# Kernel optimization log

Hardware: AMD Instinct MI355X
Metric: run time of the kernel (lower is better)

The kernel has to match this reference:

```python
import jax, jax.numpy as jnp
import numpy as np

C, H = 256, 256  # feat_num, feat_h (equirect is H x 2H)


def setup_inputs() -> dict:
    key = jax.random.key(0)
    ks = jax.random.split(key, 6)
    m = jax.random.normal(ks[0], (1, C, H, 2 * H), jnp.float32)
    b = jax.random.normal(ks[1], (1, C, H, H), jnp.float32)
    u = jax.random.normal(ks[2], (1, C, H, H), jnp.float32)
    d = jax.random.normal(ks[3], (1, C, H, H), jnp.float32)
    Wf = jax.random.normal(ks[4], (C, C, 3, 3), jnp.float32) * 0.02
    bf = jnp.zeros((C,), jnp.float32)
    Wm = jax.random.normal(ks[5], (1, 2 * C, 1, 1), jnp.float32) * 0.02
    bm = jnp.zeros((1,), jnp.float32)
    return {"m": m, "b": b, "u": u, "d": d, "Wf": Wf, "bf": bf, "Wm": Wm, "bm": bm}


def _cube2equi(cube, out_h, out_w):
    # cube: [6, C, h, h]; face order: 0 back(z-), 1 down(y-), 2 front(z+), 3 left(x-), 4 right(x+), 5 up(y+)
    h = cube.shape[-1]
    theta = (jnp.arange(out_w, dtype=cube.dtype) + 0.5) / out_w * (2.0 * jnp.pi) - jnp.pi  # longitude [-pi, pi)
    phi = jnp.pi / 2 - (jnp.arange(out_h, dtype=cube.dtype) + 0.5) / out_h * jnp.pi        # latitude [pi/2, -pi/2]
    st, ct = jnp.sin(theta)[None, :], jnp.cos(theta)[None, :]
    sp, cp = jnp.sin(phi)[:, None], jnp.cos(phi)[:, None]
    dx = cp * st
    dy = jnp.broadcast_to(sp, (out_h, out_w))
    dz = cp * ct
    ax, ay, az = jnp.abs(dx), jnp.abs(dy), jnp.abs(dz)
    mx = jnp.maximum(jnp.maximum(ax, ay), az)
    px, py, pz = dx / mx, dy / mx, dz / mx
    cond_z = (az >= ax) & (az >= ay)
    cond_x = (~cond_z) & (ax >= ay)
    face = jnp.where(cond_z, jnp.where(dz > 0, 2, 0),
           jnp.where(cond_x, jnp.where(dx > 0, 4, 3),
                              jnp.where(dy > 0, 5, 1)))
    a = jnp.where(cond_z, jnp.where(dz > 0, px, -px),
        jnp.where(cond_x, jnp.where(dx > 0, -pz, pz), px))
    bcoord = jnp.where(cond_z | cond_x, -py, jnp.where(dy > 0, pz, -pz))
    uu = jnp.clip((a + 1.0) * 0.5 * (h - 1), 0.0, h - 1)
    vv = jnp.clip((bcoord + 1.0) * 0.5 * (h - 1), 0.0, h - 1)
    u0 = jnp.floor(uu).astype(jnp.int32); v0 = jnp.floor(vv).astype(jnp.int32)
    u1 = jnp.minimum(u0 + 1, h - 1); v1 = jnp.minimum(v0 + 1, h - 1)
    wu = uu - u0; wv = vv - v0

    def samp(vi, ui):
        return cube[face, :, vi, ui]  # [out_h, out_w, C] gather over all channels

    out = (samp(v0, u0) * ((1 - wv) * (1 - wu))[..., None]
         + samp(v0, u1) * ((1 - wv) * wu)[..., None]
         + samp(v1, u0) * (wv * (1 - wu))[..., None]
         + samp(v1, u1) * (wv * wu)[..., None])
    return jnp.transpose(out, (2, 0, 1))  # [C, out_h, out_w]


def _conv(x, w, bias, pad):
    y = jax.lax.conv_general_dilated(x, w, (1, 1), [(pad, pad), (pad, pad)],
                                     dimension_numbers=("NCHW", "OIHW", "NCHW"))
    return y + bias[None, :, None, None]


def reference(m, b, u, d, Wf, bf, Wm, bm):
    h = b.shape[-1]
    empty = jnp.zeros_like(b[0])  # the torch module's zero 'emptyFace' parameter
    # faces stacked as [back, down, empty, empty, empty, up], vectorized over all channels
    cube = jnp.stack([b[0], d[0], empty, empty, empty, u[0]])  # [6, C, h, h]
    aux = _cube2equi(cube, h, 2 * h)[None]                      # [1, C, h, 2h]
    M_aux = jax.nn.relu(_conv(aux, Wf, bf, 1))
    M_main = jax.nn.relu(_conv(m, Wf, bf, 1))
    mask = jax.nn.sigmoid(_conv(jnp.concatenate([M_main, M_aux], axis=1), Wm, bm, 0))
    return m + mask * M_aux
```

## Files before the change

### kernel.cpp

```cpp
#include <hip/hip_runtime.h>
#include <hip/hip_bf16.h>

#define NPIX 131072
#define WP   514
#define XP_BYTES 67897344
#define XP_STRIDE 67962880
#define FT_BYTES 100663296

typedef __attribute__((ext_vector_type(8))) short bf16x8;
typedef __attribute__((ext_vector_type(4))) float f32x4;

typedef const __attribute__((address_space(1))) void g_cvoid;
typedef __attribute__((address_space(3))) void l_void;

__device__ __forceinline__ void async16(const void* g, void* l) {
  __builtin_amdgcn_global_load_lds((g_cvoid*)g, (l_void*)l, 16, 0, 0);
}

__global__ void zero_borders(__hip_bfloat16* Xm, __hip_bfloat16* Xa) {
  int i = blockIdx.x;
  __hip_bfloat16* X = blockIdx.y ? Xa : Xm;
  long ppix;
  if (i < 514)       ppix = i;
  else if (i < 1028) ppix = 257L * WP + (i - 514);
  else if (i < 1284) ppix = (long)(i - 1028 + 1) * WP;
  else               ppix = (long)(i - 1284 + 1) * WP + 513;
  ((unsigned int*)(X + ppix * 256))[threadIdx.x] = 0u;
}

__global__ void zero_mask(float* maskacc) {
  maskacc[blockIdx.x * 256 + threadIdx.x] = 0.f;
}

__global__ void prep_weights(const float* __restrict__ Wf, __hip_bfloat16* __restrict__ Wtt) {
  int idx = blockIdx.x * 256 + threadIdx.x;
  int cout = idx / 2304, rem = idx % 2304;
  int o = rem >> 8, ci = rem & 255;
  Wtt[(((o << 5) + (ci >> 3)) << 11) + (cout << 3) + (ci & 7)] =
      __float2bfloat16(Wf[(cout * 256 + ci) * 9 + o]);
}

__global__ void nchw_to_pad_nhwc(const float* __restrict__ src, __hip_bfloat16* __restrict__ Xp) {
  __shared__ __align__(16) __hip_bfloat16 tile[64 * 264];
  int tid = threadIdx.x;
  int p0 = blockIdx.x * 64;
  int px = tid & 63, w = tid >> 6;
  for (int k = 0; k < 64; ++k) {
    int c = (k << 2) + w;
    tile[px * 264 + c] = __float2bfloat16(src[(long)c * NPIX + p0 + px]);
  }
  __syncthreads();
  int y = p0 >> 9, x0 = p0 & 511;
  long basep = (long)(y + 1) * WP + x0 + 1;
  for (int pass = 0; pass < 8; ++pass) {
    int tpx = (pass << 3) + (tid >> 5);
    int chunk = tid & 31;
    uint4 v = *(const uint4*)&tile[tpx * 264 + (chunk << 3)];
    *(uint4*)&Xp[(basep + tpx) * 256 + (chunk << 3)] = v;
  }
}

__global__ void face_to_nhwc(const float* __restrict__ fb, const float* __restrict__ fd,
                             const float* __restrict__ fu, __hip_bfloat16* __restrict__ Ft) {
  __shared__ __align__(16) __hip_bfloat16 tile[64 * 264];
  int tid = threadIdx.x;
  int face = blockIdx.x >> 10;
  int p0 = (blockIdx.x & 1023) << 6;
  const float* src = (face == 0) ? fb : (face == 1) ? fd : fu;
  int px = tid & 63, w = tid >> 6;
  for (int k = 0; k < 64; ++k) {
    int c = (k << 2) + w;
    tile[px * 264 + c] = __float2bfloat16(src[(long)c * 65536 + p0 + px]);
  }
  __syncthreads();
  long basep = ((long)face << 16) + p0;
  for (int pass = 0; pass < 8; ++pass) {
    int tpx = (pass << 3) + (tid >> 5);
    int chunk = tid & 31;
    uint4 v = *(const uint4*)&tile[tpx * 264 + (chunk << 3)];
    *(uint4*)&Ft[((basep + tpx) << 8) + (chunk << 3)] = v;
  }
}

__device__ __forceinline__ void bf8_fma(uint4 q, float w, float* acc) {
  unsigned x;
  x = q.x; acc[0] += w * __uint_as_float(x << 16); acc[1] += w * __uint_as_float(x & 0xffff0000u);
  x = q.y; acc[2] += w * __uint_as_float(x << 16); acc[3] += w * __uint_as_float(x & 0xffff0000u);
  x = q.z; acc[4] += w * __uint_as_float(x << 16); acc[5] += w * __uint_as_float(x & 0xffff0000u);
  x = q.w; acc[6] += w * __uint_as_float(x << 16); acc[7] += w * __uint_as_float(x & 0xffff0000u);
}

__global__ void aux_gen_v2(const __hip_bfloat16* __restrict__ Ft,
                           __hip_bfloat16* __restrict__ Xp) {
  const int lane = threadIdx.x & 63;
  const int p = (blockIdx.x << 2) + (threadIdx.x >> 6);
  const int yy = p >> 9, xx = p & 511;

  float theta = ((xx + 0.5f) / 512.f) * 6.283185307179586f - 3.141592653589793f;
  float phi   = 1.5707963267948966f - ((yy + 0.5f) / 256.f) * 3.141592653589793f;
  float st = sinf(theta), ct = cosf(theta);
  float sp = sinf(phi),   cp = cosf(phi);
  float dx = cp * st, dy = sp, dz = cp * ct;
  float ax = fabsf(dx), ay = fabsf(dy), az = fabsf(dz);
  float mx = fmaxf(fmaxf(ax, ay), az);
  float pxn = dx / mx, pyn = dy / mx, pzn = dz / mx;
  bool cz = (az >= ax) && (az >= ay);
  bool cx = (!cz) && (ax >= ay);
  int face; float a, b;
  if (cz)      { face = dz > 0.f ? 2 : 0; a = dz > 0.f ? pxn : -pxn; b = -pyn; }
  else if (cx) { face = dx > 0.f ? 4 : 3; a = dx > 0.f ? -pzn : pzn; b = -pyn; }
  else         { face = dy > 0.f ? 5 : 1; a = pxn; b = dy > 0.f ? pzn : -pzn; }
  float uu = fminf(fmaxf((a + 1.f) * 0.5f * 255.f, 0.f), 255.f);
  float vv = fminf(fmaxf((b + 1.f) * 0.5f * 255.f, 0.f), 255.f);

  const long outbase = ((long)((yy + 1) * WP + xx + 1)) << 8;
  const int c0 = (lane >> 1) << 3;
  const int up = lane & 1;
  const int slot = (face == 0) ? 0 : (face == 1) ? 1 : (face == 5) ? 2 : -1;

  if (slot < 0) {
    if (!up) *(uint4*)&Xp[outbase + c0] = make_uint4(0u, 0u, 0u, 0u);
    return;
  }
  int u0 = (int)uu, v0 = (int)vv;
  int u1 = min(u0 + 1, 255), v1 = min(v0 + 1, 255);
  float wu = uu - (float)u0, wv = vv - (float)v0;
  int uc = up ? u1 : u0;
  float wA = up ? wu : (1.f - wu);
  const __hip_bfloat16* base = Ft + ((long)slot << 24);

  float acc[8] = {0.f, 0.f, 0.f, 0.f, 0.f, 0.f, 0.f, 0.f};
  uint4 q0 = *(const uint4*)&base[(((long)(v0 << 8) + uc) << 8) + c0];
  uint4 q1 = *(const uint4*)&base[(((long)(v1 << 8) + uc) << 8) + c0];
  bf8_fma(q0, (1.f - wv) * wA, acc);
  bf8_fma(q1, wv * wA, acc);
#pragma unroll
  for (int j = 0; j < 8; ++j) acc[j] += __shfl_xor(acc[j], 1);
  if (!up) {
    union { uint4 q; __hip_bfloat16 h[8]; } o;
#pragma unroll
    for (int j = 0; j < 8; ++j) o.h[j] = __float2bfloat16(acc[j]);
    *(uint4*)&Xp[outbase + c0] = o.q;
  }
}

__global__ void aux_gen(const float* __restrict__ fb, const float* __restrict__ fd,
                        const float* __restrict__ fu,
                        __hip_bfloat16* __restrict__ Xp) {
  __shared__ __align__(16) __hip_bfloat16 tile[64 * 264];
  int tid = threadIdx.x;
  int p0 = blockIdx.x * 64;
  int px = tid & 63, w = tid >> 6;

  int p = p0 + px;
  int yy = p >> 9, xx = p & 511;
  float theta = ((xx + 0.5f) / 512.f) * 6.283185307179586f - 3.141592653589793f;
  float phi   = 1.5707963267948966f - ((yy + 0.5f) / 256.f) * 3.141592653589793f;
  float st = sinf(theta), ct = cosf(theta);
  float sp = sinf(phi),   cp = cosf(phi);
  float dx = cp * st, dy = sp, dz = cp * ct;
  float ax = fabsf(dx), ay = fabsf(dy), az = fabsf(dz);
  float mx = fmaxf(fmaxf(ax, ay), az);
  float pxn = dx / mx, pyn = dy / mx, pzn = dz / mx;
  bool cz = (az >= ax) && (az >= ay);
  bool cx = (!cz) && (ax >= ay);
  int face; float a, b;
  if (cz)      { face = dz > 0.f ? 2 : 0; a = dz > 0.f ? pxn : -pxn; b = -pyn; }
  else if (cx) { face = dx > 0.f ? 4 : 3; a = dx > 0.f ? -pzn : pzn; b = -pyn; }
  else         { face = dy > 0.f ? 5 : 1; a = pxn; b = dy > 0.f ? pzn : -pzn; }
  float uu = fminf(fmaxf((a + 1.f) * 0.5f * 255.f, 0.f), 255.f);
  float vv = fminf(fmaxf((b + 1.f) * 0.5f * 255.f, 0.f), 255.f);

  const float* F = (face == 0) ? fb : (face == 1) ? fd : (face == 5) ? fu : nullptr;
  int u0 = (int)uu, v0 = (int)vv;
  int u1 = min(u0 + 1, 255), v1 = min(v0 + 1, 255);
  float wu = uu - (float)u0, wv = vv - (float)v0;
  float w00 = (1.f - wv) * (1.f - wu), w01 = (1.f - wv) * wu;
  float w10 = wv * (1.f - wu),         w11 = wv * wu;
  int i00 = v0 * 256 + u0, i01 = v0 * 256 + u1;
  int i10 = v1 * 256 + u0, i11 = v1 * 256 + u1;
  for (int k = 0; k < 64; ++k) {
    int c = (k << 2) + w;
    float val = 0.f;
    if (F) {
      const float* Fc = F + ((long)c << 16);
      val = w00 * Fc[i00] + w01 * Fc[i01] + w10 * Fc[i10] + w11 * Fc[i11];
    }
    tile[px * 264 + c] = __float2bfloat16(val);
  }
  __syncthreads();
  int y = p0 >> 9, x0g = p0 & 511;
  long basep = (long)(y + 1) * WP + x0g + 1;
  for (int pass = 0; pass < 8; ++pass) {
    int tpx = (pass << 3) + (tid >> 5);
    int chunk = tid & 31;
    uint4 v = *(const uint4*)&tile[tpx * 264 + (chunk << 3)];
    *(uint4*)&Xp[(basep + tpx) * 256 + (chunk << 3)] = v;
  }
}

template <bool STORE>
__global__ void conv3x3_mfma(const __hip_bfloat16* __restrict__ Xp,
                             const __hip_bfloat16* __restrict__ Wtt,
                             const float* __restrict__ bias,
                             const float* __restrict__ wm,
                             __hip_bfloat16* __restrict__ Out,
                             float* __restrict__ maskacc) {
  __shared__ __align__(16) __hip_bfloat16 At[4 * 80 * 32];
  const int tid = threadIdx.x;
  const int wave = tid >> 6, lane = tid & 63;
  const int bx = blockIdx.x;
  const int n0 = (bx & 1) << 7;
  const int tile = bx >> 1;
  const int x0 = (tile >> 7) << 6;
  const int y0 = (tile & 127) << 1;
  const int wrow = wave >> 1;
  const int n_off = (wave & 1) << 6;
  const int lq = lane >> 4, ln = lane & 15;

  const long stage_row = (long)(y0 + wave) * WP + x0;
  const int s_col = lane >> 2;
  const int s_ci  = (lane & 3) << 3;

  f32x4 acc[4][4] = {};

  for (int s = 0; s < 8; ++s) {
    const int ci0 = s << 5;
#pragma unroll
    for (int j = 0; j < 5; ++j) {
      const __hip_bfloat16* gp = Xp + ((stage_row + (j << 4) + s_col) << 8) + ci0 + s_ci;
      async16(gp, &At[(wave * 80 + (j << 4)) << 5]);
    }
    __syncthreads();
#pragma unroll
    for (int o = 0; o < 9; ++o) {
      const int dy = o / 3, dxo = o % 3;
      const int arow = (wrow + dy) * 80;
      bf16x8 af[4], bb[4];
#pragma unroll
      for (int mi = 0; mi < 4; ++mi)
        af[mi] = *(const bf16x8*)&At[((arow + mi * 16 + ln + dxo) << 5) + (lq << 3)];
#pragma unroll
      for (int ni = 0; ni < 4; ++ni)
        bb[ni] = *(const bf16x8*)&Wtt[(((o << 5) + (s << 2) + lq) << 11) +
                                      ((n0 + n_off + ni * 16 + ln) << 3)];
#pragma unroll
      for (int mi = 0; mi < 4; ++mi)
#pragma unroll
        for (int ni = 0; ni < 4; ++ni)
          acc[mi][ni] = __builtin_amdgcn_mfma_f32_16x16x32_bf16(af[mi], bb[ni], acc[mi][ni], 0, 0, 0);
    }
    __syncthreads();
  }

  float bv[4], wv[4];
#pragma unroll
  for (int ni = 0; ni < 4; ++ni) {
    int cc = n0 + n_off + ni * 16 + ln;
    bv[ni] = bias[cc];
    wv[ni] = wm[cc];
  }
  const int prow = (y0 + wrow) * 512 + x0;
#pragma unroll
  for (int mi = 0; mi < 4; ++mi) {
#pragma unroll
    for (int r = 0; r < 4; ++r) {
      int pix = prow + mi * 16 + (lq << 2) + r;
      float mp = 0.f;
#pragma unroll
      for (int ni = 0; ni < 4; ++ni) {
        float v = acc[mi][ni][r] + bv[ni];
        v = v > 0.f ? v : 0.f;
        if (STORE) Out[((long)pix << 8) + (n0 + n_off + ni * 16 + ln)] = __float2bfloat16(v);
        mp += v * wv[ni];
      }
      mp += __shfl_xor(mp, 1);
      mp += __shfl_xor(mp, 2);
      mp += __shfl_xor(mp, 4);
      mp += __shfl_xor(mp, 8);
      if (ln == 0) atomicAdd(&maskacc[pix], mp);
    }
  }
}

__global__ void mask_sigmoid(float* maskacc, const float* __restrict__ bm) {
  int i = blockIdx.x * 256 + threadIdx.x;
  float v = maskacc[i] + bm[0];
  maskacc[i] = 1.f / (1.f + expf(-v));
}

__global__ void final_combine(const float* __restrict__ m,
                              const __hip_bfloat16* __restrict__ MauxT,
                              const float* __restrict__ mask,
                              float* __restrict__ out) {
  __shared__ __align__(16) __hip_bfloat16 tile[64 * 264];
  __shared__ float sm[64];
  int tid = threadIdx.x;
  int p0 = blockIdx.x * 64;
  if (tid < 64) sm[tid] = mask[p0 + tid];
#pragma unroll
  for (int j = 0; j < 8; ++j) {
    int f = j * 256 + tid;
    int px = f >> 5, c8 = f & 31;
    *(uint4*)&tile[px * 264 + (c8 << 3)] =
        *(const uint4*)&MauxT[(((long)(p0 + px)) << 8) + (c8 << 3)];
  }
  __syncthreads();
  int px = tid & 63, w = tid >> 6;
  float mk = sm[px];
  for (int k = 0; k < 64; ++k) {
    int c = (k << 2) + w;
    long gi = (long)c * NPIX + p0 + px;
    out[gi] = m[gi] + mk * __bfloat162float(tile[px * 264 + c]);
  }
}

extern "C" void kernel_launch(void* const* d_in, const int* in_sizes, int n_in,
                              void* d_out, int out_size, void* d_ws, size_t ws_size,
                              hipStream_t stream) {
  const float* m  = (const float*)d_in[0];
  const float* fb = (const float*)d_in[1];
  const float* fu = (const float*)d_in[2];
  const float* fd = (const float*)d_in[3];
  const float* Wf = (const float*)d_in[4];
  const float* bf = (const float*)d_in[5];
  const float* Wm = (const float*)d_in[6];
  const float* bm = (const float*)d_in[7];
  float* out = (float*)d_out;

  char* ws = (char*)d_ws;
  const size_t NEED_FAST = (size_t)FT_BYTES + XP_STRIDE + 1179648 + 67108864 + 524288;

  if (ws_size >= NEED_FAST) {
    __hip_bfloat16* Ft     = (__hip_bfloat16*)(ws);
    __hip_bfloat16* Xp_m   = (__hip_bfloat16*)(ws);
    __hip_bfloat16* Xp_aux = (__hip_bfloat16*)(ws + (size_t)FT_BYTES);
    __hip_bfloat16* Wtt    = (__hip_bfloat16*)(ws + (size_t)FT_BYTES + XP_STRIDE);
    __hip_bfloat16* MauxT  = (__hip_bfloat16*)(ws + (size_t)FT_BYTES + XP_STRIDE + 1179648);
    float* maskacc         = (float*)(ws + (size_t)FT_BYTES + XP_STRIDE + 1179648 + 67108864);

    face_to_nhwc<<<3072, 256, 0, stream>>>(fb, fd, fu, Ft);
    aux_gen_v2<<<32768, 256, 0, stream>>>(Ft, Xp_aux);
    nchw_to_pad_nhwc<<<2048, 256, 0, stream>>>(m, Xp_m);
    zero_borders<<<dim3(1540, 2), 128, 0, stream>>>(Xp_m, Xp_aux);
    prep_weights<<<2304, 256, 0, stream>>>(Wf, Wtt);
    zero_mask<<<512, 256, 0, stream>>>(maskacc);
    conv3x3_mfma<true><<<2048, 256, 0, stream>>>(Xp_aux, Wtt, bf, Wm + 256, MauxT, maskacc);
    conv3x3_mfma<false><<<2048, 256, 0, stream>>>(Xp_m, Wtt, bf, Wm, nullptr, maskacc);
    mask_sigmoid<<<512, 256, 0, stream>>>(maskacc, bm);
    final_combine<<<2048, 256, 0, stream>>>(m, MauxT, maskacc, out);
  } else {
    __hip_bfloat16* Xp_m   = (__hip_bfloat16*)(ws);
    __hip_bfloat16* Xp_aux = (__hip_bfloat16*)(ws + (size_t)XP_STRIDE);
    __hip_bfloat16* Wtt    = (__hip_bfloat16*)(ws + 2uL * XP_STRIDE);
    __hip_bfloat16* MauxT  = (__hip_bfloat16*)(ws + 2uL * XP_STRIDE + 1179648);
    float* maskacc         = (float*)(ws + 2uL * XP_STRIDE + 1179648 + 67108864);

    zero_borders<<<dim3(1540, 2), 128, 0, stream>>>(Xp_m, Xp_aux);
    zero_mask<<<512, 256, 0, stream>>>(maskacc);
    prep_weights<<<2304, 256, 0, stream>>>(Wf, Wtt);
    nchw_to_pad_nhwc<<<2048, 256, 0, stream>>>(m, Xp_m);
    aux_gen<<<2048, 256, 0, stream>>>(fb, fd, fu, Xp_aux);
    conv3x3_mfma<true><<<2048, 256, 0, stream>>>(Xp_aux, Wtt, bf, Wm + 256, MauxT, maskacc);
    conv3x3_mfma<false><<<2048, 256, 0, stream>>>(Xp_m, Wtt, bf, Wm, nullptr, maskacc);
    mask_sigmoid<<<512, 256, 0, stream>>>(maskacc, bm);
    final_combine<<<2048, 256, 0, stream>>>(m, MauxT, maskacc, out);
  }
}
```

Baseline: 765.3 us.

## Merge both convs into one launch with 8-wave blocks covering all output channels

The two separate conv launches, one for the aux input and one for the main input, are merged into one kernel on a 2D grid where blockIdx.y selects the input. Each block grows to 512 threads (8 waves) and covers all 256 output channels, so each staged input tile in LDS is reused across every output channel instead of being loaded twice by two half-channel blocks. Tile order is also swizzled across blocks for locality. The changes aim to cut redundant input loads and launch overhead. The cost is more registers per block under launch_bounds(512,4), which may pressure occupancy or cause spills.

New measurement: 753.3 us. About the same (-1.6%).

```diff
diff --git a/kernel.cpp b/kernel.cpp
--- a/kernel.cpp
+++ b/kernel.cpp
@@ -199,26 +199,30 @@
   }
 }
 
-template <bool STORE>
-__global__ void conv3x3_mfma(const __hip_bfloat16* __restrict__ Xp,
-                             const __hip_bfloat16* __restrict__ Wtt,
-                             const float* __restrict__ bias,
-                             const float* __restrict__ wm,
-                             __hip_bfloat16* __restrict__ Out,
-                             float* __restrict__ maskacc) {
+__global__ __launch_bounds__(512, 4)
+void conv3x3_mfma(const __hip_bfloat16* __restrict__ Xpa,
+                  const __hip_bfloat16* __restrict__ Xpm,
+                  const __hip_bfloat16* __restrict__ Wtt,
+                  const float* __restrict__ bias,
+                  const float* __restrict__ wm,
+                  __hip_bfloat16* __restrict__ Out,
+                  float* __restrict__ maskacc) {
   __shared__ __align__(16) __hip_bfloat16 At[4 * 80 * 32];
   const int tid = threadIdx.x;
   const int wave = tid >> 6, lane = tid & 63;
-  const int bx = blockIdx.x;
-  const int n0 = (bx & 1) << 7;
-  const int tile = bx >> 1;
+  const bool aux = (blockIdx.y == 0);
+  const __hip_bfloat16* __restrict__ Xp = aux ? Xpa : Xpm;
+  const float* __restrict__ wmv = aux ? wm + 256 : wm;
+
+  const int tile = ((blockIdx.x & 7) << 7) + (blockIdx.x >> 3);
   const int x0 = (tile >> 7) << 6;
   const int y0 = (tile & 127) << 1;
-  const int wrow = wave >> 1;
-  const int n_off = (wave & 1) << 6;
+  const int wrow = wave >> 2;
+  const int n_off = (wave & 3) << 6;
   const int lq = lane >> 4, ln = lane & 15;
 
-  const long stage_row = (long)(y0 + wave) * WP + x0;
+  const int srow = wave >> 1;
+  const long stage_row = (long)(y0 + srow) * WP + x0;
   const int s_col = lane >> 2;
   const int s_ci  = (lane & 3) << 3;
 
@@ -226,10 +230,13 @@
 
   for (int s = 0; s < 8; ++s) {
     const int ci0 = s << 5;
-#pragma unroll
-    for (int j = 0; j < 5; ++j) {
-      const __hip_bfloat16* gp = Xp + ((stage_row + (j << 4) + s_col) << 8) + ci0 + s_ci;
-      async16(gp, &At[(wave * 80 + (j << 4)) << 5]);
+    if (wave & 1) {
+      async16(Xp + ((stage_row + 48 + s_col) << 8) + ci0 + s_ci, &At[(srow * 80 + 48) << 5]);
+      async16(Xp + ((stage_row + 64 + s_col) << 8) + ci0 + s_ci, &At[(srow * 80 + 64) << 5]);
+    } else {
+      async16(Xp + ((stage_row +  0 + s_col) << 8) + ci0 + s_ci, &At[(srow * 80 +  0) << 5]);
+      async16(Xp + ((stage_row + 16 + s_col) << 8) + ci0 + s_ci, &At[(srow * 80 + 16) << 5]);
+      async16(Xp + ((stage_row + 32 + s_col) << 8) + ci0 + s_ci, &At[(srow * 80 + 32) << 5]);
     }
     __syncthreads();
 #pragma unroll
@@ -243,7 +250,7 @@
 #pragma unroll
       for (int ni = 0; ni < 4; ++ni)
         bb[ni] = *(const bf16x8*)&Wtt[(((o << 5) + (s << 2) + lq) << 11) +
-                                      ((n0 + n_off + ni * 16 + ln) << 3)];
+                                      ((n_off + ni * 16 + ln) << 3)];
 #pragma unroll
       for (int mi = 0; mi < 4; ++mi)
 #pragma unroll
@@ -256,9 +263,9 @@
   float bv[4], wv[4];
 #pragma unroll
   for (int ni = 0; ni < 4; ++ni) {
-    int cc = n0 + n_off + ni * 16 + ln;
+    int cc = n_off + ni * 16 + ln;
     bv[ni] = bias[cc];
-    wv[ni] = wm[cc];
+    wv[ni] = wmv[cc];
   }
   const int prow = (y0 + wrow) * 512 + x0;
 #pragma unroll
@@ -271,7 +278,7 @@
       for (int ni = 0; ni < 4; ++ni) {
         float v = acc[mi][ni][r] + bv[ni];
         v = v > 0.f ? v : 0.f;
-        if (STORE) Out[((long)pix << 8) + (n0 + n_off + ni * 16 + ln)] = __float2bfloat16(v);
+        if (aux) Out[((long)pix << 8) + (n_off + ni * 16 + ln)] = __float2bfloat16(v);
         mp += v * wv[ni];
       }
       mp += __shfl_xor(mp, 1);
@@ -345,8 +352,7 @@
     zero_borders<<<dim3(1540, 2), 128, 0, stream>>>(Xp_m, Xp_aux);
     prep_weights<<<2304, 256, 0, stream>>>(Wf, Wtt);
     zero_mask<<<512, 256, 0, stream>>>(maskacc);
-    conv3x3_mfma<true><<<2048, 256, 0, stream>>>(Xp_aux, Wtt, bf, Wm + 256, MauxT, maskacc);
-    conv3x3_mfma<false><<<2048, 256, 0, stream>>>(Xp_m, Wtt, bf, Wm, nullptr, maskacc);
+    conv3x3_mfma<<<dim3(1024, 2), 512, 0, stream>>>(Xp_aux, Xp_m, Wtt, bf, Wm, MauxT, maskacc);
     mask_sigmoid<<<512, 256, 0, stream>>>(maskacc, bm);
     final_combine<<<2048, 256, 0, stream>>>(m, MauxT, maskacc, out);
   } else {
@@ -361,8 +367,7 @@
     prep_weights<<<2304, 256, 0, stream>>>(Wf, Wtt);
     nchw_to_pad_nhwc<<<2048, 256, 0, stream>>>(m, Xp_m);
     aux_gen<<<2048, 256, 0, stream>>>(fb, fd, fu, Xp_aux);
-    conv3x3_mfma<true><<<2048, 256, 0, stream>>>(Xp_aux, Wtt, bf, Wm + 256, MauxT, maskacc);
-    conv3x3_mfma<false><<<2048, 256, 0, stream>>>(Xp_m, Wtt, bf, Wm, nullptr, maskacc);
+    conv3x3_mfma<<<dim3(1024, 2), 512, 0, stream>>>(Xp_aux, Xp_m, Wtt, bf, Wm, MauxT, maskacc);
     mask_sigmoid<<<512, 256, 0, stream>>>(maskacc, bm);
     final_combine<<<2048, 256, 0, stream>>>(m, MauxT, maskacc, out);
   }
```
